# Optimization experiments

Measured on AMD Instinct MI355X. Metric: run time of the kernel, lower is better.

Reference implementation:

```python
import jax, jax.numpy as jnp
import numpy as np

B, N, F_IN, F_OUT, E = 8, 2048, 512, 256, 5
ALPHA = 0.2  # leaky relu slope
NEG = -9e15


def setup_inputs() -> dict:
    key = jax.random.key(0)
    ks = jax.random.split(key, 11)
    s_in = 1.0 / np.sqrt(F_IN)
    s_out = 1.0 / np.sqrt(F_OUT)
    s_e = 1.0 / np.sqrt(E)
    return {
        "feat": jax.random.normal(ks[0], (B, N, F_IN), jnp.float32),
        "adj": jax.random.randint(ks[1], (B, N, N), 0, 2, jnp.int32),
        "W": jax.random.normal(ks[2], (F_IN, F_OUT), jnp.float32) * s_in,
        "W_1": jax.random.normal(ks[3], (F_IN, F_OUT), jnp.float32) * s_in,
        "W_2": jax.random.normal(ks[4], (F_IN, F_OUT), jnp.float32) * s_in,
        "a_1": jax.random.normal(ks[5], (F_OUT, 1), jnp.float32) * s_out,
        "a_2": jax.random.normal(ks[6], (F_OUT, 1), jnp.float32) * s_out,
        "a_12": jax.random.normal(ks[7], (F_OUT, F_OUT), jnp.float32) * s_out,
        "L_w": jax.random.normal(ks[8], (E, F_IN), jnp.float32) * s_in,
        "R_w": jax.random.normal(ks[9], (E, F_IN), jnp.float32) * s_in,
        "B_w": jax.random.normal(ks[10], (F_OUT, E, E), jnp.float32) * s_e,
    }


def reference(feat, adj, W, W_1, W_2, a_1, a_2, a_12, L_w, R_w, B_w):
    # --- attention ---
    h = jnp.einsum('bnf,fd->bnd', feat, W)                 # [B,N,D]
    Ax = jnp.einsum('bnd,do->bno', h, a_1)[..., 0]         # [B,N] (score of target)
    Ay = jnp.einsum('bnd,do->bno', h, a_2)[..., 0]         # [B,N] (score of source)
    A_xy = jnp.einsum('bid,de,bje->bij', h, a_12, h)       # [B,N,N] bilinear term
    logits = Ax[:, None, :] + Ay[:, :, None] + A_xy        # [B,N,N]
    e = jnp.where(logits > 0, logits, ALPHA * logits)      # leaky relu
    e = jnp.where(adj > 0, e, NEG)
    attention = jax.nn.softmax(e, axis=-1)                 # dropout p=0 / eval -> identity
    # --- aggregate ---
    feat_agg = jnp.einsum('bij,bjf->bif', attention, feat) # [B,N,F_IN]
    # --- update ---
    h_1 = jnp.einsum('bnf,fd->bnd', feat, W_1)
    h_2 = jnp.einsum('bnf,fd->bnd', feat_agg, W_2)
    e1 = jnp.einsum('bnf,ef->bne', feat, L_w)              # [B,N,E]
    e2 = jnp.einsum('bnf,ef->bne', feat_agg, R_w)          # [B,N,E]
    h_12 = jnp.einsum('bni,oij,bnj->bno', e1, B_w, e2)     # [B,N,F_OUT]
    return h_1 + h_2 + h_12  # activation=None -> identity
```

## Files before the change

### kernel.cpp

```cpp
#include <hip/hip_runtime.h>
#include <hip/hip_bf16.h>

#define BB 8
#define NN 2048
#define FIN 512
#define FOUT 256
#define EE 5
#define ALPHA_ 0.2f
#define NEGV -9e15f
#define JW 512

typedef __hip_bfloat16 bf16;
typedef __bf16 bf16x8 __attribute__((ext_vector_type(8)));
typedef float f32x4 __attribute__((ext_vector_type(4)));
typedef unsigned long long u64;

__device__ __forceinline__ float bf2f(bf16 x) { return __bfloat162float(x); }
__device__ __forceinline__ bf16 f2bf(float x) { return __float2bfloat16(x); }

__device__ __forceinline__ void async16(const bf16* g, bf16* l) {
    __builtin_amdgcn_global_load_lds(
        (const __attribute__((address_space(1))) void*)g,
        (__attribute__((address_space(3))) void*)l, 16, 0, 0);
}


__global__ void split_f32_bf16(const float* __restrict__ in,
                               bf16* __restrict__ hi, bf16* __restrict__ lo) {
    long i = ((long)blockIdx.x * blockDim.x + threadIdx.x) * 8;
    float4 a = *(const float4*)(&in[i]);
    float4 b = *(const float4*)(&in[i + 4]);
    float x[8] = { a.x, a.y, a.z, a.w, b.x, b.y, b.z, b.w };
    bf16 th[8], tl[8];
    for (int k = 0; k < 8; k++) {
        th[k] = f2bf(x[k]);
        tl[k] = f2bf(x[k] - bf2f(th[k]));
    }
    *(uint4*)(&hi[i]) = *(const uint4*)th;
    *(uint4*)(&lo[i]) = *(const uint4*)tl;
}

__global__ void pack_adj(const int* __restrict__ adj, u64* __restrict__ adjm) {
    long wid = (((long)blockIdx.x * 256) + threadIdx.x) >> 6;
    int lane = threadIdx.x & 63;
    long base = wid * 256;
    for (int c = 0; c < 4; c++) {
        int a = adj[base + c * 64 + lane];
        u64 m = __ballot(a > 0);
        if (lane == 0) adjm[base / 64 + c] = m;
    }
}

__global__ void transpose_split(const float* __restrict__ in,
                                bf16* __restrict__ hi, bf16* __restrict__ lo,
                                int R, int C) {
    __shared__ bf16 th[32][33], tl[32][33];
    int c0 = blockIdx.x * 32, r0 = blockIdx.y * 32;
    int x = threadIdx.x, y = threadIdx.y;
    for (int k = 0; k < 4; k++) {
        int r = y + k * 8;
        float f = in[(long)(r0 + r) * C + c0 + x];
        bf16 h = f2bf(f);
        th[r][x] = h;
        tl[r][x] = f2bf(f - bf2f(h));
    }
    __syncthreads();
    for (int k = 0; k < 4; k++) {
        int r = y + k * 8;
        hi[(long)(c0 + r) * R + r0 + x] = th[x][r];
        lo[(long)(c0 + r) * R + r0 + x] = tl[x][r];
    }
}

__global__ void transpose_f32_bf16(const float* __restrict__ in, bf16* __restrict__ out,
                                   int R, int C, long sin_b, long sout_b) {
    __shared__ bf16 tile[32][33];
    long bi = (long)blockIdx.z * sin_b;
    long bo = (long)blockIdx.z * sout_b;
    int c0 = blockIdx.x * 32, r0 = blockIdx.y * 32;
    int x = threadIdx.x, y = threadIdx.y;
    for (int k = 0; k < 4; k++) {
        int r = y + k * 8;
        tile[r][x] = f2bf(in[bi + (long)(r0 + r) * C + c0 + x]);
    }
    __syncthreads();
    for (int k = 0; k < 4; k++) {
        int r = y + k * 8;
        out[bo + (long)(c0 + r) * R + r0 + x] = tile[x][r];
    }
}

__global__ __launch_bounds__(256) void gemm_bt_split(
        const bf16* __restrict__ Ah, const bf16* __restrict__ Al,
        const bf16* __restrict__ Bh, const bf16* __restrict__ Bl,
        bf16* __restrict__ Chi, bf16* __restrict__ Clo,
        const float* __restrict__ bias, int Nn, int K) {
    __shared__ alignas(16) bf16 Ash[128 * 32], Asl[128 * 32];
    __shared__ alignas(16) bf16 Bsh[128 * 32], Bsl[128 * 32];
    int tid = threadIdx.x;
    int lane = tid & 63, ww = tid >> 6;
    int wm = ww >> 1, wn = ww & 1;
    int quad = lane >> 4, l16 = lane & 15;
    int qx = quad ^ ((l16 >> 1) & 3);
    int sseg = (tid & 3) ^ ((tid >> 3) & 3);
    int m0 = blockIdx.x * 128, n0 = blockIdx.y * 128;
    f32x4 acc[4][4] = {};
    for (int k0 = 0; k0 < K; k0 += 32) {
#pragma unroll
        for (int i = 0; i < 2; i++) {
            int idx = tid + i * 256;
            int row = idx >> 2;
            long ao = (long)(m0 + row) * K + k0 + sseg * 8;
            long bo = (long)(n0 + row) * K + k0 + sseg * 8;
            async16(&Ah[ao], &Ash[idx * 8]);
            async16(&Al[ao], &Asl[idx * 8]);
            async16(&Bh[bo], &Bsh[idx * 8]);
            async16(&Bl[bo], &Bsl[idx * 8]);
        }
        __syncthreads();
        bf16x8 afh[4], afl[4], bfh[4], bfl[4];
        for (int mi = 0; mi < 4; mi++) {
            int so = (wm * 64 + mi * 16 + l16) * 32 + qx * 8;
            afh[mi] = *(const bf16x8*)(&Ash[so]);
            afl[mi] = *(const bf16x8*)(&Asl[so]);
        }
        for (int ni = 0; ni < 4; ni++) {
            int so = (wn * 64 + ni * 16 + l16) * 32 + qx * 8;
            bfh[ni] = *(const bf16x8*)(&Bsh[so]);
            bfl[ni] = *(const bf16x8*)(&Bsl[so]);
        }
        for (int mi = 0; mi < 4; mi++)
            for (int ni = 0; ni < 4; ni++) {
                acc[mi][ni] = __builtin_amdgcn_mfma_f32_16x16x32_bf16(afh[mi], bfh[ni], acc[mi][ni], 0, 0, 0);
                acc[mi][ni] = __builtin_amdgcn_mfma_f32_16x16x32_bf16(afh[mi], bfl[ni], acc[mi][ni], 0, 0, 0);
                acc[mi][ni] = __builtin_amdgcn_mfma_f32_16x16x32_bf16(afl[mi], bfh[ni], acc[mi][ni], 0, 0, 0);
            }
        __syncthreads();
    }
    for (int mi = 0; mi < 4; mi++)
        for (int ni = 0; ni < 4; ni++) {
            int col = n0 + wn * 64 + ni * 16 + l16;
            float bv = bias ? bias[col] : 0.f;
            for (int r = 0; r < 4; r++) {
                int row = m0 + wm * 64 + mi * 16 + quad * 4 + r;
                float v = acc[mi][ni][r] + bv;
                bf16 h = f2bf(v);
                Chi[(long)row * Nn + col] = h;
                Clo[(long)row * Nn + col] = f2bf(v - bf2f(h));
            }
        }
}

__global__ __launch_bounds__(256) void gemm_bt(
        const bf16* __restrict__ A, const bf16* __restrict__ Bt,
        bf16* __restrict__ C, int Nn, int K, long sA, long sB, long sC) {
    __shared__ alignas(16) bf16 As[128 * 32];
    __shared__ alignas(16) bf16 Bs[128 * 32];
    const bf16* Ab = A + (long)blockIdx.z * sA;
    const bf16* Bb = Bt + (long)blockIdx.z * sB;
    bf16* Cb = C + (long)blockIdx.z * sC;
    int tid = threadIdx.x;
    int lane = tid & 63, ww = tid >> 6;
    int wm = ww >> 1, wn = ww & 1;
    int quad = lane >> 4, l16 = lane & 15;
    int qx = quad ^ ((l16 >> 1) & 3);
    int sseg = (tid & 3) ^ ((tid >> 3) & 3);
    int m0 = blockIdx.x * 128, n0 = blockIdx.y * 128;
    f32x4 acc[4][4] = {};
    for (int k0 = 0; k0 < K; k0 += 32) {
#pragma unroll
        for (int i = 0; i < 2; i++) {
            int idx = tid + i * 256;
            int row = idx >> 2;
            async16(&Ab[(long)(m0 + row) * K + k0 + sseg * 8], &As[idx * 8]);
            async16(&Bb[(long)(n0 + row) * K + k0 + sseg * 8], &Bs[idx * 8]);
        }
        __syncthreads();
        bf16x8 af[4], bfr[4];
        for (int mi = 0; mi < 4; mi++)
            af[mi] = *(const bf16x8*)(&As[(wm * 64 + mi * 16 + l16) * 32 + qx * 8]);
        for (int ni = 0; ni < 4; ni++)
            bfr[ni] = *(const bf16x8*)(&Bs[(wn * 64 + ni * 16 + l16) * 32 + qx * 8]);
        for (int mi = 0; mi < 4; mi++)
            for (int ni = 0; ni < 4; ni++)
                acc[mi][ni] = __builtin_amdgcn_mfma_f32_16x16x32_bf16(
                    af[mi], bfr[ni], acc[mi][ni], 0, 0, 0);
        __syncthreads();
    }
    for (int mi = 0; mi < 4; mi++)
        for (int ni = 0; ni < 4; ni++) {
            int col = n0 + wn * 64 + ni * 16 + l16;
            for (int r = 0; r < 4; r++) {
                int row = m0 + wm * 64 + mi * 16 + quad * 4 + r;
                Cb[(long)row * Nn + col] = f2bf(acc[mi][ni][r]);
            }
        }
}

__global__ __launch_bounds__(256) void gemm_pv(
        const bf16* __restrict__ A, const bf16* __restrict__ Bt,
        bf16* __restrict__ C, const float* __restrict__ rs,
        const float* __restrict__ fin) {
    __shared__ alignas(16) bf16 As[128 * 32];
    __shared__ alignas(16) bf16 Bs[128 * 32];
    int b = blockIdx.z;
    const bf16* Ab = A + (long)b * NN * NN;
    const bf16* Bb = Bt + (long)b * FIN * NN;
    bf16* Cb = C + (long)b * NN * FIN;
    int tid = threadIdx.x;
    int lane = tid & 63, ww = tid >> 6;
    int wm = ww >> 1, wn = ww & 1;
    int quad = lane >> 4, l16 = lane & 15;
    int qx = quad ^ ((l16 >> 1) & 3);
    int sseg = (tid & 3) ^ ((tid >> 3) & 3);
    int m0 = blockIdx.x * 128, n0 = blockIdx.y * 128;
    f32x4 acc[4][4] = {};
    for (int k0 = 0; k0 < NN; k0 += 32) {
        if (k0 && !(k0 & 127)) {
            int c = k0 >> 7;
#pragma unroll
            for (int mi = 0; mi < 4; mi++) {
                float4 rv = *(const float4*)(&rs[((long)b * 16 + c) * NN
                                                 + m0 + wm * 64 + mi * 16 + quad * 4]);
#pragma unroll
                for (int ni = 0; ni < 4; ni++) {
                    acc[mi][ni][0] *= rv.x;
                    acc[mi][ni][1] *= rv.y;
                    acc[mi][ni][2] *= rv.z;
                    acc[mi][ni][3] *= rv.w;
                }
            }
        }
#pragma unroll
        for (int i = 0; i < 2; i++) {
            int idx = tid + i * 256;
            int row = idx >> 2;
            async16(&Ab[(long)(m0 + row) * NN + k0 + sseg * 8], &As[idx * 8]);
            async16(&Bb[(long)(n0 + row) * NN + k0 + sseg * 8], &Bs[idx * 8]);
        }
        __syncthreads();
        bf16x8 af[4], bfr[4];
        for (int mi = 0; mi < 4; mi++)
            af[mi] = *(const bf16x8*)(&As[(wm * 64 + mi * 16 + l16) * 32 + qx * 8]);
        for (int ni = 0; ni < 4; ni++)
            bfr[ni] = *(const bf16x8*)(&Bs[(wn * 64 + ni * 16 + l16) * 32 + qx * 8]);
        for (int mi = 0; mi < 4; mi++)
            for (int ni = 0; ni < 4; ni++)
                acc[mi][ni] = __builtin_amdgcn_mfma_f32_16x16x32_bf16(
                    af[mi], bfr[ni], acc[mi][ni], 0, 0, 0);
        __syncthreads();
    }
    for (int mi = 0; mi < 4; mi++) {
        float4 fv = *(const float4*)(&fin[(long)b * NN + m0 + wm * 64 + mi * 16 + quad * 4]);
        for (int ni = 0; ni < 4; ni++) {
            int col = n0 + wn * 64 + ni * 16 + l16;
            float fvr[4] = { fv.x, fv.y, fv.z, fv.w };
            for (int r = 0; r < 4; r++) {
                int row = m0 + wm * 64 + mi * 16 + quad * 4 + r;
                Cb[(long)row * FIN + col] = f2bf(acc[mi][ni][r] * fvr[r]);
            }
        }
    }
}

__global__ void ay_kernel(const bf16* __restrict__ hh, const bf16* __restrict__ hl,
                          const float* __restrict__ a2, float* __restrict__ Ay) {
    int lane = threadIdx.x & 63, w = threadIdx.x >> 6;
    long row = (long)blockIdx.x * 4 + w;
    float p = 0.f;
    for (int i = 0; i < 4; i++) {
        int d = i * 64 + lane;
        p += (bf2f(hh[row * FOUT + d]) + bf2f(hl[row * FOUT + d])) * a2[d];
    }
    for (int off = 32; off; off >>= 1) p += __shfl_xor(p, off);
    if (lane == 0) Ay[row] = p;
}

__global__ __launch_bounds__(256, 2) void pass_score(
        const bf16* __restrict__ qh_, const bf16* __restrict__ ql_,
        const bf16* __restrict__ hh_, const bf16* __restrict__ hl_,
        const u64* __restrict__ adjm, const float* __restrict__ Ay,
        float* __restrict__ mpm, float* __restrict__ mpl,
        bf16* __restrict__ P) {
    __shared__ alignas(16) bf16 Hsh[2][128 * 32], Hsl[2][128 * 32];
    __shared__ alignas(16) bf16 pst[4][16 * 64];
    int tid = threadIdx.x;
    int lane = tid & 63, w = tid >> 6;
    int quad = lane >> 4, l16 = lane & 15;
    int qx = quad ^ ((l16 >> 1) & 3);
    int sseg = (tid & 3) ^ ((tid >> 3) & 3);
    int b = blockIdx.z, jz = blockIdx.y;
    int iw = blockIdx.x * 128 + w * 32;
    const bf16* hbh = hh_ + ((long)b * NN + (long)jz * JW) * FOUT;
    const bf16* hbl = hl_ + ((long)b * NN + (long)jz * JW) * FOUT;
    const u64* amb = adjm + ((long)b * NN + iw) * (NN / 64) + jz * (JW / 64);
    bf16* pw = pst[w];

    bf16x8 qfh[2][8], qfl[2][8];
#pragma unroll
    for (int mi = 0; mi < 2; mi++) {
        long qoff = ((long)b * NN + iw + mi * 16 + l16) * FOUT;
#pragma unroll
        for (int kk = 0; kk < 8; kk++) {
            qfh[mi][kk] = *(const bf16x8*)(&qh_[qoff + kk * 32 + quad * 8]);
            qfl[mi][kk] = *(const bf16x8*)(&ql_[qoff + kk * 32 + quad * 8]);
        }
    }
    float ay_[2][4];
#pragma unroll
    for (int mi = 0; mi < 2; mi++)
#pragma unroll
        for (int r = 0; r < 4; r++)
            ay_[mi][r] = Ay[(long)b * NN + iw + mi * 16 + quad * 4 + r];

    float m_[2][4], l_[2][4];
#pragma unroll
    for (int mi = 0; mi < 2; mi++)
#pragma unroll
        for (int r = 0; r < 4; r++) { m_[mi][r] = -3.0e38f; l_[mi][r] = 0.f; }

    auto STAGE = [&](int jc, int kk, int buf) {
#pragma unroll
        for (int i = 0; i < 2; i++) {
            int idx = tid + i * 256;
            int row = idx >> 2;
            long go = (long)(jc * 128 + row) * FOUT + kk * 32 + sseg * 8;
            async16(&hbh[go], &Hsh[buf][idx * 8]);
            async16(&hbl[go], &Hsl[buf][idx * 8]);
        }
    };

    f32x4 sacc[2][8];
#pragma unroll
    for (int mi = 0; mi < 2; mi++)
#pragma unroll
        for (int ni = 0; ni < 8; ni++) sacc[mi][ni] = (f32x4){0.f, 0.f, 0.f, 0.f};

    STAGE(0, 0, 0);
    for (int jc = 0; jc < 4; jc++) {
#pragma unroll
        for (int kk = 0; kk < 8; kk++) {
            const int cur = kk & 1;
            if (kk < 7)           STAGE(jc, kk + 1, cur ^ 1);
            else if (jc < 3)      STAGE(jc + 1, 0, cur ^ 1);
            if (kk == 0) {
                if (jc == 0) asm volatile("s_waitcnt vmcnt(4)" ::: "memory");
                else         asm volatile("s_waitcnt vmcnt(20)" ::: "memory");
            } else if (kk == 7 && jc == 3) {
                asm volatile("s_waitcnt vmcnt(0)" ::: "memory");
            } else {
                asm volatile("s_waitcnt vmcnt(4)" ::: "memory");
            }
            __builtin_amdgcn_s_barrier();
            __builtin_amdgcn_sched_barrier(0);

            __builtin_amdgcn_s_setprio(1);
#pragma unroll
            for (int ni = 0; ni < 8; ni++) {
                int so = (ni * 16 + l16) * 32 + qx * 8;
                bf16x8 hfh = *(const bf16x8*)(&Hsh[cur][so]);
                bf16x8 hfl = *(const bf16x8*)(&Hsl[cur][so]);
#pragma unroll
                for (int mi = 0; mi < 2; mi++) {
                    sacc[mi][ni] = __builtin_amdgcn_mfma_f32_16x16x32_bf16(qfh[mi][kk], hfh, sacc[mi][ni], 0, 0, 0);
                    sacc[mi][ni] = __builtin_amdgcn_mfma_f32_16x16x32_bf16(qfh[mi][kk], hfl, sacc[mi][ni], 0, 0, 0);
                    sacc[mi][ni] = __builtin_amdgcn_mfma_f32_16x16x32_bf16(qfl[mi][kk], hfh, sacc[mi][ni], 0, 0, 0);
                }
            }
            __builtin_amdgcn_s_setprio(0);

            if (kk == 7) {
#pragma unroll
                for (int mi = 0; mi < 2; mi++) {
                    u64 am[4][2];
#pragma unroll
                    for (int r = 0; r < 4; r++) {
                        long ro = (long)(mi * 16 + quad * 4 + r) * (NN / 64) + jc * 2;
                        am[r][0] = amb[ro + 0];
                        am[r][1] = amb[ro + 1];
                    }
#pragma unroll
                    for (int ni = 0; ni < 8; ni++)
#pragma unroll
                        for (int r = 0; r < 4; r++) {
                            float v = sacc[mi][ni][r] + ay_[mi][r];
                            v = v > 0.f ? v : ALPHA_ * v;
                            int bit = (int)((am[r][ni >> 2] >> ((ni * 16 + l16) & 63)) & 1);
                            sacc[mi][ni][r] = bit ? v : NEGV;
                        }
#pragma unroll
                    for (int r = 0; r < 4; r++) {
                        float mc = -3.0e38f;
#pragma unroll
                        for (int ni = 0; ni < 8; ni++) mc = fmaxf(mc, sacc[mi][ni][r]);
                        for (int off = 8; off; off >>= 1) mc = fmaxf(mc, __shfl_xor(mc, off));
                        float mnew = fmaxf(m_[mi][r], mc);
                        float scale = __expf(m_[mi][r] - mnew);
                        float ps = 0.f;
#pragma unroll
                        for (int ni = 0; ni < 8; ni++) {
                            float p = __expf(sacc[mi][ni][r] - mnew);
                            sacc[mi][ni][r] = p;
                            ps += p;
                        }
                        for (int off = 8; off; off >>= 1) ps += __shfl_xor(ps, off);
                        l_[mi][r] = l_[mi][r] * scale + ps;
                        m_[mi][r] = mnew;
                        if (l16 == 0)
                            mpm[(((long)b * 4 + jz) * 4 + jc) * NN + iw + mi * 16 + quad * 4 + r] = mnew;
                    }
#pragma unroll
                    for (int h = 0; h < 2; h++) {
#pragma unroll
                        for (int ni = 0; ni < 4; ni++)
#pragma unroll
                            for (int r = 0; r < 4; r++) {
                                int row = quad * 4 + r;
                                int byt = (row * 128 + (ni * 16 + l16) * 2) ^ ((row & 7) << 4);
                                *(bf16*)((char*)pw + byt) = f2bf(sacc[mi][h * 4 + ni][r]);
                            }
#pragma unroll
                        for (int s2 = 0; s2 < 2; s2++) {
                            int cq = quad + s2 * 4;
                            int byt = (l16 * 128 + cq * 16) ^ ((l16 & 7) << 4);
                            uint4 v = *(const uint4*)((const char*)pw + byt);
                            *(uint4*)(&P[((long)b * NN + iw + mi * 16 + l16) * NN + (long)jz * JW
                                         + jc * 128 + h * 64 + cq * 8]) = v;
                        }
                    }
#pragma unroll
                    for (int ni = 0; ni < 8; ni++) sacc[mi][ni] = (f32x4){0.f, 0.f, 0.f, 0.f};
                }
            }
            __builtin_amdgcn_sched_barrier(0);
            __builtin_amdgcn_s_barrier();
            __builtin_amdgcn_sched_barrier(0);
        }
    }
    if (l16 == 0)
#pragma unroll
        for (int mi = 0; mi < 2; mi++)
#pragma unroll
            for (int r = 0; r < 4; r++)
                mpl[((long)b * 4 + jz) * NN + iw + mi * 16 + quad * 4 + r] = l_[mi][r];
}

__global__ void ml_merge(const float* __restrict__ mpm, const float* __restrict__ mpl,
                         float* __restrict__ rs, float* __restrict__ fin) {
    long row = (long)blockIdx.x * blockDim.x + threadIdx.x;
    long b = row / NN, n = row % NN;
    float mc[16];
#pragma unroll
    for (int c = 0; c < 16; c++) mc[c] = mpm[(b * 16 + c) * NN + n];
    float m = fmaxf(fmaxf(mc[3], mc[7]), fmaxf(mc[11], mc[15]));
    float l = 0.f;
#pragma unroll
    for (int jz = 0; jz < 4; jz++)
        l += mpl[(b * 4 + jz) * NN + n] * __expf(mc[jz * 4 + 3] - m);
    fin[row] = __expf(mc[15] - m) / l;
#pragma unroll
    for (int c = 1; c < 16; c++)
        rs[(b * 16 + c) * NN + n] = __expf(mc[c - 1] - mc[c]);
}

__global__ void e_kernel(const bf16* __restrict__ X, const float* __restrict__ Wt,
                         float* __restrict__ out) {
    int lane = threadIdx.x & 63, w = threadIdx.x >> 6;
    long row = (long)blockIdx.x * 4 + w;
    uint4 raw = *(const uint4*)(&X[row * FIN + lane * 8]);
    const bf16* xp = (const bf16*)&raw;
    float xv[8];
    for (int i = 0; i < 8; i++) xv[i] = bf2f(xp[i]);
    for (int e = 0; e < EE; e++) {
        float4 w0 = *(const float4*)(&Wt[e * FIN + lane * 8]);
        float4 w1 = *(const float4*)(&Wt[e * FIN + lane * 8 + 4]);
        float p = xv[0] * w0.x + xv[1] * w0.y + xv[2] * w0.z + xv[3] * w0.w
                + xv[4] * w1.x + xv[5] * w1.y + xv[6] * w1.z + xv[7] * w1.w;
        for (int off = 32; off; off >>= 1) p += __shfl_xor(p, off);
        if (lane == 0) out[row * EE + e] = p;
    }
}

__global__ void final_kernel(float* __restrict__ out,
                             const bf16* __restrict__ h1, const bf16* __restrict__ h2,
                             const float* __restrict__ e1, const float* __restrict__ e2,
                             const float* __restrict__ Bw) {
    long row = blockIdx.x;
    int o = threadIdx.x;
    float a[EE], c[EE];
    for (int i = 0; i < EE; i++) { a[i] = e1[row * EE + i]; c[i] = e2[row * EE + i]; }
    const float* bw = Bw + (long)o * EE * EE;
    float acc = 0.f;
    for (int i = 0; i < EE; i++)
        for (int j = 0; j < EE; j++)
            acc += bw[i * EE + j] * a[i] * c[j];
    long idx = row * FOUT + o;
    out[idx] = acc + bf2f(h1[idx]) + bf2f(h2[idx]);
}

extern "C" void kernel_launch(void* const* d_in, const int* in_sizes, int n_in,
                              void* d_out, int out_size, void* d_ws, size_t ws_size,
                              hipStream_t stream) {
    const float* feat = (const float*)d_in[0];
    const int*   adj  = (const int*)d_in[1];
    const float* W    = (const float*)d_in[2];
    const float* W1   = (const float*)d_in[3];
    const float* W2   = (const float*)d_in[4];
    const float* a1   = (const float*)d_in[5];
    const float* a2   = (const float*)d_in[6];
    const float* a12  = (const float*)d_in[7];
    const float* Lw   = (const float*)d_in[8];
    const float* Rw   = (const float*)d_in[9];
    const float* Bw   = (const float*)d_in[10];
    float* out = (float*)d_out;

    char* ws = (char*)d_ws;
    size_t off = 0;
    auto alloc = [&](size_t bytes) {
        char* p = ws + off;
        off += (bytes + 255) & ~(size_t)255;
        return p;
    };
    bf16* WTh  = (bf16*)alloc((size_t)FOUT * FIN * 2);
    bf16* WTl  = (bf16*)alloc((size_t)FOUT * FIN * 2);
    bf16* W1T  = (bf16*)alloc((size_t)FOUT * FIN * 2);
    bf16* W2T  = (bf16*)alloc((size_t)FOUT * FIN * 2);
    bf16* aTh  = (bf16*)alloc((size_t)FOUT * FOUT * 2);
    bf16* aTl  = (bf16*)alloc((size_t)FOUT * FOUT * 2);
    bf16* fh   = (bf16*)alloc((size_t)BB * NN * FIN * 2);
    bf16* fl   = (bf16*)alloc((size_t)BB * NN * FIN * 2);
    bf16* hh   = (bf16*)alloc((size_t)BB * NN * FOUT * 2);
    bf16* hl   = (bf16*)alloc((size_t)BB * NN * FOUT * 2);
    bf16* featT= (bf16*)alloc((size_t)BB * NN * FIN * 2);
    float* Ay  = (float*)alloc((size_t)BB * NN * 4);
    float* mpm = (float*)alloc((size_t)BB * 4 * 4 * NN * 4);
    float* mpl = (float*)alloc((size_t)BB * 4 * NN * 4);
    float* rs  = (float*)alloc((size_t)BB * 16 * NN * 4);
    float* fin = (float*)alloc((size_t)BB * NN * 4);
    float* e1  = (float*)alloc((size_t)BB * NN * EE * 4);
    float* e2  = (float*)alloc((size_t)BB * NN * EE * 4);
    u64* adjm  = (u64*)alloc((size_t)BB * NN * (NN / 64) * 8);
    bf16* P    = (bf16*)alloc((size_t)BB * NN * NN * 2);
    bf16* qh   = (bf16*)d_out;
    bf16* ql   = qh + (size_t)BB * NN * FOUT;
    bf16* fagg = fl;
    bf16* h1   = hh;
    bf16* h2   = hl;

    dim3 tb(32, 8, 1);
    split_f32_bf16<<<(BB * NN * FIN) / (256 * 8), 256, 0, stream>>>(feat, fh, fl);
    pack_adj<<<(BB * NN * NN) / (256 * 4), 256, 0, stream>>>(adj, adjm);
    transpose_split<<<dim3(FOUT / 32, FIN / 32, 1), tb, 0, stream>>>(W, WTh, WTl, FIN, FOUT);
    transpose_split<<<dim3(FOUT / 32, FOUT / 32, 1), tb, 0, stream>>>(a12, aTh, aTl, FOUT, FOUT);
    transpose_f32_bf16<<<dim3(FOUT / 32, FIN / 32, 1), tb, 0, stream>>>(W1, W1T, FIN, FOUT, 0, 0);
    transpose_f32_bf16<<<dim3(FOUT / 32, FIN / 32, 1), tb, 0, stream>>>(W2, W2T, FIN, FOUT, 0, 0);
    transpose_f32_bf16<<<dim3(FIN / 32, NN / 32, BB), tb, 0, stream>>>(
        feat, featT, NN, FIN, (long)NN * FIN, (long)FIN * NN);
    gemm_bt_split<<<dim3(BB * NN / 128, FOUT / 128, 1), 256, 0, stream>>>(
        fh, fl, WTh, WTl, hh, hl, nullptr, FOUT, FIN);
    ay_kernel<<<BB * NN / 4, 256, 0, stream>>>(hh, hl, a2, Ay);
    gemm_bt_split<<<dim3(BB * NN / 128, FOUT / 128, 1), 256, 0, stream>>>(
        hh, hl, aTh, aTl, qh, ql, a1, FOUT, FOUT);
    pass_score<<<dim3(NN / 128, 4, BB), 256, 0, stream>>>(
        qh, ql, hh, hl, adjm, Ay, mpm, mpl, P);
    ml_merge<<<(BB * NN) / 256, 256, 0, stream>>>(mpm, mpl, rs, fin);
    gemm_pv<<<dim3(NN / 128, FIN / 128, BB), 256, 0, stream>>>(
        P, featT, fagg, rs, fin);
    gemm_bt<<<dim3(BB * NN / 128, FOUT / 128, 1), 256, 0, stream>>>(
        fh, W1T, h1, FOUT, FIN, 0, 0, 0);
    gemm_bt<<<dim3(BB * NN / 128, FOUT / 128, 1), 256, 0, stream>>>(
        fagg, W2T, h2, FOUT, FIN, 0, 0, 0);
    e_kernel<<<BB * NN / 4, 256, 0, stream>>>(fh, Lw, e1);
    e_kernel<<<BB * NN / 4, 256, 0, stream>>>(fagg, Rw, e2);
    final_kernel<<<BB * NN, FOUT, 0, stream>>>(out, h1, h2, e1, e2, Bw);
}
```

Baseline: 549.4 us.

## Halve pass_score row tile, triple-buffer H staging, drop second barrier

Each wave in the attention score kernel now handles 16 query rows instead of 32, and the grid doubles to keep total work the same. The H-tile staging moves from double to triple buffering with a prefetch distance of two, so the trailing per-iteration barrier can be removed. Adjacency mask loads are hoisted to the start of each column chunk. This is meant to raise occupancy and overlap loads with compute, at the cost of reloading each staged H tile for twice as many blocks and fewer MFMAs per LDS read.

After: 530.2 us. 3.5% less time.

```diff
diff --git a/kernel.cpp b/kernel.cpp
--- a/kernel.cpp
+++ b/kernel.cpp
@@ -276,48 +276,40 @@
     if (lane == 0) Ay[row] = p;
 }
 
-__global__ __launch_bounds__(256, 2) void pass_score(
+__global__ __launch_bounds__(256) void pass_score(
         const bf16* __restrict__ qh_, const bf16* __restrict__ ql_,
         const bf16* __restrict__ hh_, const bf16* __restrict__ hl_,
         const u64* __restrict__ adjm, const float* __restrict__ Ay,
         float* __restrict__ mpm, float* __restrict__ mpl,
         bf16* __restrict__ P) {
-    __shared__ alignas(16) bf16 Hsh[2][128 * 32], Hsl[2][128 * 32];
-    __shared__ alignas(16) bf16 pst[4][16 * 64];
+    __shared__ alignas(16) bf16 Hsh[3 * 128 * 32], Hsl[3 * 128 * 32];
+    __shared__ alignas(16) bf16 pst[4][16 * 32];
     int tid = threadIdx.x;
     int lane = tid & 63, w = tid >> 6;
     int quad = lane >> 4, l16 = lane & 15;
     int qx = quad ^ ((l16 >> 1) & 3);
     int sseg = (tid & 3) ^ ((tid >> 3) & 3);
     int b = blockIdx.z, jz = blockIdx.y;
-    int iw = blockIdx.x * 128 + w * 32;
+    int i0 = blockIdx.x * 64 + w * 16;
+    long qoff = ((long)b * NN + i0) * FOUT;
     const bf16* hbh = hh_ + ((long)b * NN + (long)jz * JW) * FOUT;
     const bf16* hbl = hl_ + ((long)b * NN + (long)jz * JW) * FOUT;
-    const u64* amb = adjm + ((long)b * NN + iw) * (NN / 64) + jz * (JW / 64);
-    bf16* pw = pst[w];
-
-    bf16x8 qfh[2][8], qfl[2][8];
-#pragma unroll
-    for (int mi = 0; mi < 2; mi++) {
-        long qoff = ((long)b * NN + iw + mi * 16 + l16) * FOUT;
-#pragma unroll
-        for (int kk = 0; kk < 8; kk++) {
-            qfh[mi][kk] = *(const bf16x8*)(&qh_[qoff + kk * 32 + quad * 8]);
-            qfl[mi][kk] = *(const bf16x8*)(&ql_[qoff + kk * 32 + quad * 8]);
-        }
-    }
-    float ay_[2][4];
-#pragma unroll
-    for (int mi = 0; mi < 2; mi++)
-#pragma unroll
-        for (int r = 0; r < 4; r++)
-            ay_[mi][r] = Ay[(long)b * NN + iw + mi * 16 + quad * 4 + r];
-
-    float m_[2][4], l_[2][4];
-#pragma unroll
-    for (int mi = 0; mi < 2; mi++)
-#pragma unroll
-        for (int r = 0; r < 4; r++) { m_[mi][r] = -3.0e38f; l_[mi][r] = 0.f; }
+    const u64* amb = adjm + ((long)b * NN + i0) * (NN / 64) + jz * (JW / 64);
+    char* pwc = (char*)pst[w];
+
+    bf16x8 qfh[8], qfl[8];
+#pragma unroll
+    for (int kk = 0; kk < 8; kk++) {
+        qfh[kk] = *(const bf16x8*)(&qh_[qoff + (long)l16 * FOUT + kk * 32 + quad * 8]);
+        qfl[kk] = *(const bf16x8*)(&ql_[qoff + (long)l16 * FOUT + kk * 32 + quad * 8]);
+    }
+    float ay_[4];
+#pragma unroll
+    for (int r = 0; r < 4; r++) ay_[r] = Ay[(long)b * NN + i0 + quad * 4 + r];
+
+    float m_[4], l_[4];
+#pragma unroll
+    for (int r = 0; r < 4; r++) { m_[r] = -3.0e38f; l_[r] = 0.f; }
 
     auto STAGE = [&](int jc, int kk, int buf) {
 #pragma unroll
@@ -325,27 +317,32 @@
             int idx = tid + i * 256;
             int row = idx >> 2;
             long go = (long)(jc * 128 + row) * FOUT + kk * 32 + sseg * 8;
-            async16(&hbh[go], &Hsh[buf][idx * 8]);
-            async16(&hbl[go], &Hsl[buf][idx * 8]);
+            async16(&hbh[go], &Hsh[buf * 4096 + idx * 8]);
+            async16(&hbl[go], &Hsl[buf * 4096 + idx * 8]);
         }
     };
 
-    f32x4 sacc[2][8];
-#pragma unroll
-    for (int mi = 0; mi < 2; mi++)
-#pragma unroll
-        for (int ni = 0; ni < 8; ni++) sacc[mi][ni] = (f32x4){0.f, 0.f, 0.f, 0.f};
+    f32x4 sacc[8];
+#pragma unroll
+    for (int ni = 0; ni < 8; ni++) sacc[ni] = (f32x4){0.f, 0.f, 0.f, 0.f};
 
     STAGE(0, 0, 0);
+    STAGE(0, 1, 1);
+    int c0 = 0;
     for (int jc = 0; jc < 4; jc++) {
+        u64 am[4][2];
 #pragma unroll
         for (int kk = 0; kk < 8; kk++) {
-            const int cur = kk & 1;
-            if (kk < 7)           STAGE(jc, kk + 1, cur ^ 1);
-            else if (jc < 3)      STAGE(jc + 1, 0, cur ^ 1);
+            int cur = c0 + (kk % 3);       if (cur >= 3) cur -= 3;
+            int nxt = c0 + ((kk + 2) % 3); if (nxt >= 3) nxt -= 3;
             if (kk == 0) {
                 if (jc == 0) asm volatile("s_waitcnt vmcnt(4)" ::: "memory");
+                else         asm volatile("s_waitcnt vmcnt(12)" ::: "memory");
+            } else if (kk == 1) {
+                if (jc == 0) asm volatile("s_waitcnt vmcnt(12)" ::: "memory");
                 else         asm volatile("s_waitcnt vmcnt(20)" ::: "memory");
+            } else if (kk == 2) {
+                asm volatile("s_waitcnt vmcnt(12)" ::: "memory");
             } else if (kk == 7 && jc == 3) {
                 asm volatile("s_waitcnt vmcnt(0)" ::: "memory");
             } else {
@@ -353,96 +350,86 @@
             }
             __builtin_amdgcn_s_barrier();
             __builtin_amdgcn_sched_barrier(0);
+            if (kk < 6)       STAGE(jc, kk + 2, nxt);
+            else if (jc < 3)  STAGE(jc + 1, kk - 6, nxt);
+            if (kk == 0) {
+#pragma unroll
+                for (int r = 0; r < 4; r++) {
+                    long ro = (long)(quad * 4 + r) * (NN / 64) + jc * 2;
+                    am[r][0] = amb[ro + 0];
+                    am[r][1] = amb[ro + 1];
+                }
+            }
 
             __builtin_amdgcn_s_setprio(1);
 #pragma unroll
             for (int ni = 0; ni < 8; ni++) {
-                int so = (ni * 16 + l16) * 32 + qx * 8;
-                bf16x8 hfh = *(const bf16x8*)(&Hsh[cur][so]);
-                bf16x8 hfl = *(const bf16x8*)(&Hsl[cur][so]);
-#pragma unroll
-                for (int mi = 0; mi < 2; mi++) {
-                    sacc[mi][ni] = __builtin_amdgcn_mfma_f32_16x16x32_bf16(qfh[mi][kk], hfh, sacc[mi][ni], 0, 0, 0);
-                    sacc[mi][ni] = __builtin_amdgcn_mfma_f32_16x16x32_bf16(qfh[mi][kk], hfl, sacc[mi][ni], 0, 0, 0);
-                    sacc[mi][ni] = __builtin_amdgcn_mfma_f32_16x16x32_bf16(qfl[mi][kk], hfh, sacc[mi][ni], 0, 0, 0);
+                int so = cur * 4096 + (ni * 16 + l16) * 32 + qx * 8;
+                bf16x8 hfh = *(const bf16x8*)(&Hsh[so]);
+                bf16x8 hfl = *(const bf16x8*)(&Hsl[so]);
+                sacc[ni] = __builtin_amdgcn_mfma_f32_16x16x32_bf16(qfh[kk], hfh, sacc[ni], 0, 0, 0);
+                sacc[ni] = __builtin_amdgcn_mfma_f32_16x16x32_bf16(qfh[kk], hfl, sacc[ni], 0, 0, 0);
+                sacc[ni] = __builtin_amdgcn_mfma_f32_16x16x32_bf16(qfl[kk], hfh, sacc[ni], 0, 0, 0);
+            }
+            __builtin_amdgcn_s_setprio(0);
+
+            if (kk == 7) {
+#pragma unroll
+                for (int ni = 0; ni < 8; ni++)
+#pragma unroll
+                    for (int r = 0; r < 4; r++) {
+                        float v = sacc[ni][r] + ay_[r];
+                        v = v > 0.f ? v : ALPHA_ * v;
+                        int bit = (int)((am[r][ni >> 2] >> ((ni * 16 + l16) & 63)) & 1);
+                        sacc[ni][r] = bit ? v : NEGV;
+                    }
+#pragma unroll
+                for (int r = 0; r < 4; r++) {
+                    float mc = -3.0e38f;
+#pragma unroll
+                    for (int ni = 0; ni < 8; ni++) mc = fmaxf(mc, sacc[ni][r]);
+                    for (int off = 8; off; off >>= 1) mc = fmaxf(mc, __shfl_xor(mc, off));
+                    float mnew = fmaxf(m_[r], mc);
+                    float scale = __expf(m_[r] - mnew);
+                    float ps = 0.f;
+#pragma unroll
+                    for (int ni = 0; ni < 8; ni++) {
+                        float p = __expf(sacc[ni][r] - mnew);
+                        sacc[ni][r] = p;
+                        ps += p;
+                    }
+                    for (int off = 8; off; off >>= 1) ps += __shfl_xor(ps, off);
+                    l_[r] = l_[r] * scale + ps;
+                    m_[r] = mnew;
+                    if (l16 == 0)
+                        mpm[(((long)b * 4 + jz) * 4 + jc) * NN + i0 + quad * 4 + r] = mnew;
                 }
-            }
-            __builtin_amdgcn_s_setprio(0);
-
-            if (kk == 7) {
-#pragma unroll
-                for (int mi = 0; mi < 2; mi++) {
-                    u64 am[4][2];
-#pragma unroll
-                    for (int r = 0; r < 4; r++) {
-                        long ro = (long)(mi * 16 + quad * 4 + r) * (NN / 64) + jc * 2;
-                        am[r][0] = amb[ro + 0];
-                        am[r][1] = amb[ro + 1];
-                    }
-#pragma unroll
-                    for (int ni = 0; ni < 8; ni++)
+#pragma unroll
+                for (int qi = 0; qi < 4; qi++) {
+#pragma unroll
+                    for (int ni2 = 0; ni2 < 2; ni2++)
 #pragma unroll
                         for (int r = 0; r < 4; r++) {
-                            float v = sacc[mi][ni][r] + ay_[mi][r];
-                            v = v > 0.f ? v : ALPHA_ * v;
-                            int bit = (int)((am[r][ni >> 2] >> ((ni * 16 + l16) & 63)) & 1);
-                            sacc[mi][ni][r] = bit ? v : NEGV;
+                            int row = quad * 4 + r;
+                            int byt = (row * 64 + ni2 * 32 + l16 * 2) ^ ((row & 7) << 4);
+                            *(bf16*)(pwc + byt) = f2bf(sacc[qi * 2 + ni2][r]);
                         }
-#pragma unroll
-                    for (int r = 0; r < 4; r++) {
-                        float mc = -3.0e38f;
-#pragma unroll
-                        for (int ni = 0; ni < 8; ni++) mc = fmaxf(mc, sacc[mi][ni][r]);
-                        for (int off = 8; off; off >>= 1) mc = fmaxf(mc, __shfl_xor(mc, off));
-                        float mnew = fmaxf(m_[mi][r], mc);
-                        float scale = __expf(m_[mi][r] - mnew);
-                        float ps = 0.f;
-#pragma unroll
-                        for (int ni = 0; ni < 8; ni++) {
-                            float p = __expf(sacc[mi][ni][r] - mnew);
-                            sacc[mi][ni][r] = p;
-                            ps += p;
-                        }
-                        for (int off = 8; off; off >>= 1) ps += __shfl_xor(ps, off);
-                        l_[mi][r] = l_[mi][r] * scale + ps;
-                        m_[mi][r] = mnew;
-                        if (l16 == 0)
-                            mpm[(((long)b * 4 + jz) * 4 + jc) * NN + iw + mi * 16 + quad * 4 + r] = mnew;
-                    }
-#pragma unroll
-                    for (int h = 0; h < 2; h++) {
-#pragma unroll
-                        for (int ni = 0; ni < 4; ni++)
-#pragma unroll
-                            for (int r = 0; r < 4; r++) {
-                                int row = quad * 4 + r;
-                                int byt = (row * 128 + (ni * 16 + l16) * 2) ^ ((row & 7) << 4);
-                                *(bf16*)((char*)pw + byt) = f2bf(sacc[mi][h * 4 + ni][r]);
-                            }
-#pragma unroll
-                        for (int s2 = 0; s2 < 2; s2++) {
-                            int cq = quad + s2 * 4;
-                            int byt = (l16 * 128 + cq * 16) ^ ((l16 & 7) << 4);
-                            uint4 v = *(const uint4*)((const char*)pw + byt);
-                            *(uint4*)(&P[((long)b * NN + iw + mi * 16 + l16) * NN + (long)jz * JW
-                                         + jc * 128 + h * 64 + cq * 8]) = v;
-                        }
-                    }
-#pragma unroll
-                    for (int ni = 0; ni < 8; ni++) sacc[mi][ni] = (f32x4){0.f, 0.f, 0.f, 0.f};
+                    int byt = (l16 * 64 + quad * 16) ^ ((l16 & 7) << 4);
+                    uint4 v = *(const uint4*)(pwc + byt);
+                    *(uint4*)(&P[((long)b * NN + i0 + l16) * NN + (long)jz * JW
+                                 + jc * 128 + qi * 32 + quad * 8]) = v;
                 }
+#pragma unroll
+                for (int ni = 0; ni < 8; ni++) sacc[ni] = (f32x4){0.f, 0.f, 0.f, 0.f};
             }
             __builtin_amdgcn_sched_barrier(0);
-            __builtin_amdgcn_s_barrier();
-            __builtin_amdgcn_sched_barrier(0);
-        }
+        }
+        c0 += 2; if (c0 >= 3) c0 -= 3;
     }
     if (l16 == 0)
 #pragma unroll
-        for (int mi = 0; mi < 2; mi++)
-#pragma unroll
-            for (int r = 0; r < 4; r++)
-                mpl[((long)b * 4 + jz) * NN + iw + mi * 16 + quad * 4 + r] = l_[mi][r];
+        for (int r = 0; r < 4; r++)
+            mpl[((long)b * 4 + jz) * NN + i0 + quad * 4 + r] = l_[r];
 }
 
 __global__ void ml_merge(const float* __restrict__ mpm, const float* __restrict__ mpl,
@@ -561,7 +548,7 @@
     ay_kernel<<<BB * NN / 4, 256, 0, stream>>>(hh, hl, a2, Ay);
     gemm_bt_split<<<dim3(BB * NN / 128, FOUT / 128, 1), 256, 0, stream>>>(
         hh, hl, aTh, aTl, qh, ql, a1, FOUT, FOUT);
-    pass_score<<<dim3(NN / 128, 4, BB), 256, 0, stream>>>(
+    pass_score<<<dim3(NN / 64, 4, BB), 256, 0, stream>>>(
         qh, ql, hh, hl, adjm, Ay, mpm, mpl, P);
     ml_merge<<<(BB * NN) / 256, 256, 0, stream>>>(mpm, mpl, rs, fin);
     gemm_pv<<<dim3(NN / 128, FIN / 128, BB), 256, 0, stream>>>(
```
